# Performance work log

Measured on AMD Instinct MI355X. Metric: run time of the kernel, lower is better.

## Reference

```python
import jax, jax.numpy as jnp
import numpy as np
import math

NUM_LABELS = 8
D_MODEL = 1024
NUM_HEADS = 16
D_PADDED = math.ceil(D_MODEL / NUM_HEADS) * NUM_HEADS  # 1024
D_HEAD = D_PADDED // NUM_HEADS  # 64
B, N = 4, 2048


def setup_inputs() -> dict:
    key = jax.random.key(0)
    ks = jax.random.split(key, 7)
    X = jax.random.normal(ks[0], (B, N, D_MODEL), dtype=jnp.float32)
    L = jax.random.randint(ks[1], (B, N), 0, NUM_LABELS, dtype=jnp.int32)
    # per-label QKV linear params (stored as x @ W + b layout)
    s_in = 1.0 / math.sqrt(D_MODEL)
    Wqkv = jax.random.uniform(ks[2], (NUM_LABELS, D_MODEL, 3 * D_PADDED), jnp.float32, -s_in, s_in)
    bqkv = jax.random.uniform(ks[3], (NUM_LABELS, 3 * D_PADDED), jnp.float32, -s_in, s_in)
    s_p = 1.0 / math.sqrt(D_PADDED)
    Wproj = jax.random.uniform(ks[4], (D_PADDED, D_MODEL), jnp.float32, -s_p, s_p)
    bproj = jax.random.uniform(ks[5], (D_MODEL,), jnp.float32, -s_p, s_p)
    return {"X": X, "L": L, "Wqkv": Wqkv, "bqkv": bqkv, "Wproj": Wproj, "bproj": bproj}


def reference(X, L, Wqkv, bqkv, Wproj, bproj):
    Bb, Nn, _ = X.shape
    # Per-label dense QKV projection, routed by label mask (matches original
    # per-label loop; X_masked zeroing is a no-op on selected positions).
    qkv = jnp.zeros((Bb, Nn, 3 * D_PADDED), dtype=X.dtype)
    for l in range(NUM_LABELS):
        m = (L == l)[..., None]  # [B, N, 1]
        qkv_l = jnp.einsum('bnd,do->bno', X, Wqkv[l]) + bqkv[l]
        qkv = jnp.where(m, qkv_l, qkv)
    q, k, v = jnp.split(qkv, 3, axis=-1)
    # [B, H, N, Dh]
    q = q.reshape(Bb, Nn, NUM_HEADS, D_HEAD).transpose(0, 2, 1, 3)
    k = k.reshape(Bb, Nn, NUM_HEADS, D_HEAD).transpose(0, 2, 1, 3)
    v = v.reshape(Bb, Nn, NUM_HEADS, D_HEAD).transpose(0, 2, 1, 3)
    scores = jnp.einsum('bhnd,bhmd->bhnm', q, k) / math.sqrt(D_HEAD)
    probs = jax.nn.softmax(scores, axis=-1)
    out = jnp.einsum('bhnm,bhmd->bhnd', probs, v)
    out = out.transpose(0, 2, 1, 3).reshape(Bb, Nn, D_PADDED)
    return jnp.einsum('bnd,do->bno', out, Wproj) + bproj
```

## Files before the change

kernel.cpp:

```cpp
#include <hip/hip_runtime.h>
#include <math.h>

#define BATCH 4
#define SEQ   2048
#define TOK   (BATCH * SEQ)
#define DM    1024
#define DP    1024
#define NH    16
#define DH    64
#define NLAB  8
#define QKV_C 3072
#define PADL  1152
#define PROWS (NLAB * PADL)
#define GP    72

typedef __attribute__((ext_vector_type(8))) short bf16x8;
typedef __attribute__((ext_vector_type(4))) float f32x4;

__device__ __forceinline__ short f2bf(float f) {
  union { float f; unsigned u; } v; v.f = f;
  unsigned r = v.u + 0x7FFF + ((v.u >> 16) & 1);
  return (short)(r >> 16);
}

__device__ __forceinline__ unsigned cvt_pk_bf16(float lo, float hi) {
  unsigned r;
  asm("v_cvt_pk_bf16_f32 %0, %1, %2" : "=v"(r) : "v"(lo), "v"(hi));
  return r;
}

__device__ __forceinline__ float fast_exp2(float x) {
#if __has_builtin(__builtin_amdgcn_exp2f)
  return __builtin_amdgcn_exp2f(x);
#else
  return exp2f(x);
#endif
}

__global__ void build_lists_k(const int* __restrict__ L, int* __restrict__ sorted,
                              int* __restrict__ rowmap) {
  __shared__ int cnt[NLAB], off[NLAB], cur[NLAB];
  int tid = threadIdx.x;
  if (tid < NLAB) cnt[tid] = 0;
  __syncthreads();
  for (int i = tid; i < TOK; i += 256) atomicAdd(&cnt[L[i]], 1);
  __syncthreads();
  if (tid == 0) {
    int o = 0;
    for (int l = 0; l < NLAB; ++l) { off[l] = o; cur[l] = o; o += cnt[l]; }
  }
  __syncthreads();
  for (int i = tid; i < TOK; i += 256) {
    int l = L[i];
    sorted[atomicAdd(&cur[l], 1)] = i;
  }
  __threadfence();
  __syncthreads();
  for (int p = tid; p < PROWS; p += 256) {
    int l = p / PADL, i = p - l * PADL;
    rowmap[p] = (i < cnt[l]) ? sorted[off[l] + i] : -1;
  }
}

__global__ __launch_bounds__(256) void xg_k(const float* __restrict__ X,
                                            const int* __restrict__ rowmap,
                                            short* __restrict__ Xg) {
  int p = blockIdx.x;
  int t = rowmap[p];
  int c = threadIdx.x << 2;
  short* dst = Xg + (size_t)p * DM + c;
  if (t >= 0) {
    float4 v = *(const float4*)(X + (size_t)t * DM + c);
    short tmp[4] = { f2bf(v.x), f2bf(v.y), f2bf(v.z), f2bf(v.w) };
    *(uint2*)dst = *(uint2*)tmp;
  } else {
    uint2 z; z.x = 0u; z.y = 0u;
    *(uint2*)dst = z;
  }
}

__global__ __launch_bounds__(256) void wt_k(const float* __restrict__ src,
                                            short* __restrict__ dst,
                                            int K, int N) {
  __shared__ float Ts[64][65];
  int m = blockIdx.z;
  src += (size_t)m * K * N;
  dst += (size_t)m * (size_t)N * K;
  int n0 = blockIdx.x * 64, k0 = blockIdx.y * 64;
  int tid = threadIdx.x;
  int r = tid >> 4;
  int c = (tid & 15) << 2;
  #pragma unroll
  for (int it = 0; it < 4; ++it) {
    float4 v = *(const float4*)(src + (size_t)(k0 + r + it * 16) * N + n0 + c);
    Ts[c + 0][r + it * 16] = v.x;
    Ts[c + 1][r + it * 16] = v.y;
    Ts[c + 2][r + it * 16] = v.z;
    Ts[c + 3][r + it * 16] = v.w;
  }
  __syncthreads();
  int n = tid >> 2, ks = (tid & 3) << 4;
  short tmp[16];
  #pragma unroll
  for (int j = 0; j < 16; ++j) tmp[j] = f2bf(Ts[n][ks + j]);
  *(bf16x8*)(dst + (size_t)(n0 + n) * K + k0 + ks)     = *(bf16x8*)&tmp[0];
  *(bf16x8*)(dst + (size_t)(n0 + n) * K + k0 + ks + 8) = *(bf16x8*)&tmp[8];
}

__global__ __launch_bounds__(256) void qkv_mfma_k(
    const short* __restrict__ Xg, const short* __restrict__ Wt,
    const float* __restrict__ bqkv, const int* __restrict__ rowmap,
    short* __restrict__ qkvb) {
  __shared__ short As[128 * GP];
  __shared__ short Bs[128 * GP];
  int bx = blockIdx.x, by = blockIdx.y;
  int lab = by / 9;
  int pr0 = by * 128;
  int n0  = bx * 128;
  const short* W = Wt + (size_t)lab * QKV_C * DM;

  int tid  = threadIdx.x;
  int lane = tid & 63, w = tid >> 6;
  int wm = w >> 1, wn = w & 1;
  int col = lane & 15, quad = lane >> 4;

  int srow = tid >> 2;
  int scol = (tid & 3) << 4;

  const short* a0 = Xg + (size_t)(pr0 + srow) * DM + scol;
  const short* a1 = Xg + (size_t)(pr0 + 64 + srow) * DM + scol;
  const short* b0 = W + (size_t)(n0 + srow) * DM + scol;
  const short* b1 = W + (size_t)(n0 + 64 + srow) * DM + scol;

  f32x4 acc[4][4];
  #pragma unroll
  for (int mi = 0; mi < 4; ++mi)
    #pragma unroll
    for (int ni = 0; ni < 4; ++ni) acc[mi][ni] = (f32x4){0.f, 0.f, 0.f, 0.f};

  bf16x8 ra[4], rb[4];
  ra[0] = *(const bf16x8*)(a0);     ra[1] = *(const bf16x8*)(a0 + 8);
  ra[2] = *(const bf16x8*)(a1);     ra[3] = *(const bf16x8*)(a1 + 8);
  rb[0] = *(const bf16x8*)(b0);     rb[1] = *(const bf16x8*)(b0 + 8);
  rb[2] = *(const bf16x8*)(b1);     rb[3] = *(const bf16x8*)(b1 + 8);

  for (int k0 = 0; k0 < DM; k0 += 64) {
    *(bf16x8*)&As[srow * GP + scol]            = ra[0];
    *(bf16x8*)&As[srow * GP + scol + 8]        = ra[1];
    *(bf16x8*)&As[(64 + srow) * GP + scol]     = ra[2];
    *(bf16x8*)&As[(64 + srow) * GP + scol + 8] = ra[3];
    *(bf16x8*)&Bs[srow * GP + scol]            = rb[0];
    *(bf16x8*)&Bs[srow * GP + scol + 8]        = rb[1];
    *(bf16x8*)&Bs[(64 + srow) * GP + scol]     = rb[2];
    *(bf16x8*)&Bs[(64 + srow) * GP + scol + 8] = rb[3];
    __syncthreads();
    if (k0 + 64 < DM) {
      int kn = k0 + 64;
      ra[0] = *(const bf16x8*)(a0 + kn);     ra[1] = *(const bf16x8*)(a0 + kn + 8);
      ra[2] = *(const bf16x8*)(a1 + kn);     ra[3] = *(const bf16x8*)(a1 + kn + 8);
      rb[0] = *(const bf16x8*)(b0 + kn);     rb[1] = *(const bf16x8*)(b0 + kn + 8);
      rb[2] = *(const bf16x8*)(b1 + kn);     rb[3] = *(const bf16x8*)(b1 + kn + 8);
    }
    #pragma unroll
    for (int ks = 0; ks < 2; ++ks) {
      bf16x8 a[4], b[4];
      #pragma unroll
      for (int mi = 0; mi < 4; ++mi)
        a[mi] = *(bf16x8*)&As[(wm * 64 + mi * 16 + col) * GP + ks * 32 + (quad << 3)];
      #pragma unroll
      for (int ni = 0; ni < 4; ++ni)
        b[ni] = *(bf16x8*)&Bs[(wn * 64 + ni * 16 + col) * GP + ks * 32 + (quad << 3)];
      #pragma unroll
      for (int mi = 0; mi < 4; ++mi)
        #pragma unroll
        for (int ni = 0; ni < 4; ++ni)
          acc[mi][ni] = __builtin_amdgcn_mfma_f32_16x16x32_bf16(a[mi], b[ni], acc[mi][ni], 0, 0, 0);
    }
    __syncthreads();
  }

  float scale = (bx < 8) ? (0.125f * 1.44269504f) : 1.0f;
  const float* bias = bqkv + lab * QKV_C;
  #pragma unroll
  for (int mi = 0; mi < 4; ++mi) {
    #pragma unroll
    for (int r = 0; r < 4; ++r) {
      int prow = pr0 + wm * 64 + mi * 16 + (quad << 2) + r;
      int t2 = rowmap[prow];
      if (t2 < 0) continue;
      #pragma unroll
      for (int ni = 0; ni < 4; ++ni) {
        int gn = n0 + wn * 64 + ni * 16 + col;
        float v = (acc[mi][ni][r] + bias[gn]) * scale;
        qkvb[(size_t)t2 * QKV_C + gn] = f2bf(v);
      }
    }
  }
}

__global__ __launch_bounds__(256) void vtb_k(const short* __restrict__ qkvb,
                                             short* __restrict__ VTg) {
  __shared__ short T[64 * GP];
  int n0 = blockIdx.x * 64, h = blockIdx.y, b = blockIdx.z;
  int tid = threadIdx.x;
  int r = tid >> 2, cb = tid & 3;
  {
    const short* src = qkvb + ((size_t)(b * SEQ + n0 + r)) * QKV_C + 2 * DP + h * DH + (cb << 4);
    int scc = ((cb + (r >> 4)) & 3) << 4;
    *(bf16x8*)&T[r * GP + scc]     = *(const bf16x8*)(src);
    *(bf16x8*)&T[r * GP + scc + 8] = *(const bf16x8*)(src + 8);
  }
  __syncthreads();
  int d = tid >> 2, nc = (tid & 3) << 4;
  int sc2 = (((d >> 4) + (nc >> 4)) & 3) << 4;
  short tmp[16];
  #pragma unroll
  for (int j = 0; j < 16; ++j) tmp[j] = T[(nc + j) * GP + sc2 + (d & 15)];
  short* dst = VTg + ((size_t)(b * NH + h) * DH + d) * SEQ + n0 + nc;
  *(bf16x8*)&dst[0] = *(bf16x8*)&tmp[0];
  *(bf16x8*)&dst[8] = *(bf16x8*)&tmp[8];
}

__global__ __launch_bounds__(256) void attn_k(short* __restrict__ qkvb,
                                              const short* __restrict__ VTg) {
  int qt = blockIdx.x, h = blockIdx.y, b = blockIdx.z;
  __shared__ short Ks[64 * GP];
  __shared__ short VT[64 * GP];
  __shared__ short Ps[128 * GP];

  int tid  = threadIdx.x;
  int lane = tid & 63;
  int w    = tid >> 6;
  int col  = lane & 15;
  int quad = lane >> 4;

  size_t rowbase = (size_t)b * SEQ;
  int hoff = h * DH;
  int sr = tid >> 2;
  int sc = (tid & 3) << 4;

  const short* ksrc = qkvb + (rowbase + sr) * QKV_C + DP + hoff + sc;
  const short* vsrc = VTg + ((size_t)(b * NH + h) * DH + sr) * SEQ + sc;

  bf16x8 qf0[2], qf1[2];
  {
    const short* q0 = qkvb + (rowbase + qt * 128 + (w << 4) + col) * QKV_C + hoff + (quad << 3);
    const short* q1 = q0 + (size_t)64 * QKV_C;
    qf0[0] = *(const bf16x8*)(q0);
    qf0[1] = *(const bf16x8*)(q0 + 32);
    qf1[0] = *(const bf16x8*)(q1);
    qf1[1] = *(const bf16x8*)(q1 + 32);
  }

  {
    bf16x8 ka = *(const bf16x8*)(ksrc);
    bf16x8 kb = *(const bf16x8*)(ksrc + 8);
    bf16x8 va = *(const bf16x8*)(vsrc);
    bf16x8 vb = *(const bf16x8*)(vsrc + 8);
    *(bf16x8*)&Ks[sr * GP + sc]     = ka;
    *(bf16x8*)&Ks[sr * GP + sc + 8] = kb;
    *(bf16x8*)&VT[sr * GP + sc]     = va;
    *(bf16x8*)&VT[sr * GP + sc + 8] = vb;
  }
  __syncthreads();

  float m_0 = -1e30f, l_0 = 0.f, m_1 = -1e30f, l_1 = 0.f;
  f32x4 o0[4], o1[4];
  #pragma unroll
  for (int nd = 0; nd < 4; ++nd) {
    o0[nd] = (f32x4){0.f, 0.f, 0.f, 0.f};
    o1[nd] = (f32x4){0.f, 0.f, 0.f, 0.f};
  }

  short* ps0 = &Ps[((w << 4) + col) * GP];
  short* ps1 = &Ps[(64 + (w << 4) + col) * GP];

  auto softmax_strip = [&](f32x4* s, float& m_, float& l_, f32x4* o, short* psrow) {
    f32x4 t0, t1;
    #pragma unroll
    for (int i = 0; i < 4; ++i) { t0[i] = fmaxf(s[0][i], s[1][i]); t1[i] = fmaxf(s[2][i], s[3][i]); }
    #pragma unroll
    for (int i = 0; i < 4; ++i) t0[i] = fmaxf(t0[i], t1[i]);
    float mx = fmaxf(fmaxf(t0[0], t0[1]), fmaxf(t0[2], t0[3]));
    if (!__all(mx - m_ <= 8.f)) {
      float mxr = fmaxf(mx, __shfl_xor(mx, 16));
      mxr = fmaxf(mxr, __shfl_xor(mxr, 32));
      float mnew  = fmaxf(m_, mxr);
      float alpha = fast_exp2(m_ - mnew);
      l_ *= alpha;
      #pragma unroll
      for (int nd = 0; nd < 4; ++nd)
        #pragma unroll
        for (int r = 0; r < 4; ++r) o[nd][r] *= alpha;
      m_ = mnew;
    }
    float p[4][4];
    #pragma unroll
    for (int nj = 0; nj < 4; ++nj)
      #pragma unroll
      for (int r = 0; r < 4; ++r) p[nj][r] = fast_exp2(s[nj][r] - m_);
    float rs = 0.f;
    #pragma unroll
    for (int nj = 0; nj < 4; ++nj)
      rs += (p[nj][0] + p[nj][1]) + (p[nj][2] + p[nj][3]);
    l_ += rs;
    #pragma unroll
    for (int nj = 0; nj < 4; ++nj) {
      uint2 u;
      u.x = cvt_pk_bf16(p[nj][0], p[nj][1]);
      u.y = cvt_pk_bf16(p[nj][2], p[nj][3]);
      *(uint2*)&psrow[nj * 16 + (quad << 2)] = u;
    }
  };

  auto compute_tile = [&]() {
    f32x4 s0[4], s1[4];
    #pragma unroll
    for (int nj = 0; nj < 4; ++nj) {
      s0[nj] = (f32x4){0.f, 0.f, 0.f, 0.f};
      s1[nj] = (f32x4){0.f, 0.f, 0.f, 0.f};
    }
    __builtin_amdgcn_s_setprio(1);
    #pragma unroll
    for (int ks = 0; ks < 2; ++ks) {
      #pragma unroll
      for (int nj = 0; nj < 4; ++nj) {
        bf16x8 aK = *(bf16x8*)&Ks[((nj << 4) + col) * GP + (ks << 5) + (quad << 3)];
        s0[nj] = __builtin_amdgcn_mfma_f32_16x16x32_bf16(aK, qf0[ks], s0[nj], 0, 0, 0);
        s1[nj] = __builtin_amdgcn_mfma_f32_16x16x32_bf16(aK, qf1[ks], s1[nj], 0, 0, 0);
      }
    }
    __builtin_amdgcn_s_setprio(0);
    softmax_strip(s0, m_0, l_0, o0, ps0);
    softmax_strip(s1, m_1, l_1, o1, ps1);
    __builtin_amdgcn_s_setprio(1);
    #pragma unroll
    for (int ks = 0; ks < 2; ++ks) {
      bf16x8 bP0 = *(bf16x8*)&ps0[(ks << 5) + (quad << 3)];
      bf16x8 bP1 = *(bf16x8*)&ps1[(ks << 5) + (quad << 3)];
      #pragma unroll
      for (int nd = 0; nd < 4; ++nd) {
        bf16x8 aV = *(bf16x8*)&VT[((nd << 4) + col) * GP + (ks << 5) + (quad << 3)];
        o0[nd] = __builtin_amdgcn_mfma_f32_16x16x32_bf16(aV, bP0, o0[nd], 0, 0, 0);
        o1[nd] = __builtin_amdgcn_mfma_f32_16x16x32_bf16(aV, bP1, o1[nd], 0, 0, 0);
      }
    }
    __builtin_amdgcn_s_setprio(0);
  };

  for (int kt = 0; kt < SEQ / 64 - 1; ++kt) {
    const short* kn = ksrc + (size_t)(kt + 1) * 64 * QKV_C;
    const short* vn = vsrc + (size_t)(kt + 1) * 64;
    bf16x8 ka = *(const bf16x8*)(kn);
    bf16x8 kb = *(const bf16x8*)(kn + 8);
    bf16x8 va = *(const bf16x8*)(vn);
    bf16x8 vb = *(const bf16x8*)(vn + 8);

    compute_tile();
    __syncthreads();
    *(bf16x8*)&Ks[sr * GP + sc]     = ka;
    *(bf16x8*)&Ks[sr * GP + sc + 8] = kb;
    *(bf16x8*)&VT[sr * GP + sc]     = va;
    *(bf16x8*)&VT[sr * GP + sc + 8] = vb;
    __syncthreads();
  }
  compute_tile();

  float lt0 = l_0 + __shfl_xor(l_0, 16);
  lt0 += __shfl_xor(lt0, 32);
  float lt1 = l_1 + __shfl_xor(l_1, 16);
  lt1 += __shfl_xor(lt1, 32);
  #pragma unroll
  for (int s = 0; s < 2; ++s) {
    float inv = 1.f / (s ? lt1 : lt0);
    f32x4* o = s ? o1 : o0;
    size_t row = rowbase + qt * 128 + s * 64 + (w << 4) + col;
    #pragma unroll
    for (int nd = 0; nd < 4; ++nd) {
      uint2 u;
      u.x = cvt_pk_bf16(o[nd][0] * inv, o[nd][1] * inv);
      u.y = cvt_pk_bf16(o[nd][2] * inv, o[nd][3] * inv);
      *(uint2*)(qkvb + row * QKV_C + hoff + (nd << 4) + (quad << 2)) = u;
    }
  }
}

__global__ __launch_bounds__(256) void proj_mfma_k(
    const short* __restrict__ Ab, const short* __restrict__ Wt,
    const float* __restrict__ bias, float* __restrict__ out) {
  __shared__ short As[128 * GP];
  __shared__ short Bs[128 * GP];
  int n0 = blockIdx.x * 128, m0 = blockIdx.y * 128;

  int tid  = threadIdx.x;
  int lane = tid & 63, w = tid >> 6;
  int wm = w >> 1, wn = w & 1;
  int col = lane & 15, quad = lane >> 4;
  int srow = tid >> 2;
  int scol = (tid & 3) << 4;

  const short* a0 = Ab + (size_t)(m0 + srow) * QKV_C + scol;
  const short* a1 = Ab + (size_t)(m0 + 64 + srow) * QKV_C + scol;
  const short* b0 = Wt + (size_t)(n0 + srow) * DP + scol;
  const short* b1 = Wt + (size_t)(n0 + 64 + srow) * DP + scol;

  f32x4 acc[4][4];
  #pragma unroll
  for (int mi = 0; mi < 4; ++mi)
    #pragma unroll
    for (int ni = 0; ni < 4; ++ni) acc[mi][ni] = (f32x4){0.f, 0.f, 0.f, 0.f};

  bf16x8 ra[4], rb[4];
  ra[0] = *(const bf16x8*)(a0);     ra[1] = *(const bf16x8*)(a0 + 8);
  ra[2] = *(const bf16x8*)(a1);     ra[3] = *(const bf16x8*)(a1 + 8);
  rb[0] = *(const bf16x8*)(b0);     rb[1] = *(const bf16x8*)(b0 + 8);
  rb[2] = *(const bf16x8*)(b1);     rb[3] = *(const bf16x8*)(b1 + 8);

  for (int k0 = 0; k0 < DP; k0 += 64) {
    *(bf16x8*)&As[srow * GP + scol]            = ra[0];
    *(bf16x8*)&As[srow * GP + scol + 8]        = ra[1];
    *(bf16x8*)&As[(64 + srow) * GP + scol]     = ra[2];
    *(bf16x8*)&As[(64 + srow) * GP + scol + 8] = ra[3];
    *(bf16x8*)&Bs[srow * GP + scol]            = rb[0];
    *(bf16x8*)&Bs[srow * GP + scol + 8]        = rb[1];
    *(bf16x8*)&Bs[(64 + srow) * GP + scol]     = rb[2];
    *(bf16x8*)&Bs[(64 + srow) * GP + scol + 8] = rb[3];
    __syncthreads();
    if (k0 + 64 < DP) {
      int kn = k0 + 64;
      ra[0] = *(const bf16x8*)(a0 + kn);     ra[1] = *(const bf16x8*)(a0 + kn + 8);
      ra[2] = *(const bf16x8*)(a1 + kn);     ra[3] = *(const bf16x8*)(a1 + kn + 8);
      rb[0] = *(const bf16x8*)(b0 + kn);     rb[1] = *(const bf16x8*)(b0 + kn + 8);
      rb[2] = *(const bf16x8*)(b1 + kn);     rb[3] = *(const bf16x8*)(b1 + kn + 8);
    }
    #pragma unroll
    for (int ks = 0; ks < 2; ++ks) {
      bf16x8 a[4], b[4];
      #pragma unroll
      for (int mi = 0; mi < 4; ++mi)
        a[mi] = *(bf16x8*)&As[(wm * 64 + mi * 16 + col) * GP + ks * 32 + (quad << 3)];
      #pragma unroll
      for (int ni = 0; ni < 4; ++ni)
        b[ni] = *(bf16x8*)&Bs[(wn * 64 + ni * 16 + col) * GP + ks * 32 + (quad << 3)];
      #pragma unroll
      for (int mi = 0; mi < 4; ++mi)
        #pragma unroll
        for (int ni = 0; ni < 4; ++ni)
          acc[mi][ni] = __builtin_amdgcn_mfma_f32_16x16x32_bf16(a[mi], b[ni], acc[mi][ni], 0, 0, 0);
    }
    __syncthreads();
  }

  #pragma unroll
  for (int mi = 0; mi < 4; ++mi) {
    #pragma unroll
    for (int r = 0; r < 4; ++r) {
      int m = m0 + wm * 64 + mi * 16 + (quad << 2) + r;
      #pragma unroll
      for (int ni = 0; ni < 4; ++ni) {
        int gn = n0 + wn * 64 + ni * 16 + col;
        out[(size_t)m * DM + gn] = acc[mi][ni][r] + bias[gn];
      }
    }
  }
}

extern "C" void kernel_launch(void* const* d_in, const int* in_sizes, int n_in,
                              void* d_out, int out_size, void* d_ws, size_t ws_size,
                              hipStream_t stream) {
  (void)in_sizes; (void)n_in; (void)out_size; (void)ws_size;
  const float* X     = (const float*)d_in[0];
  const int*   L     = (const int*)d_in[1];
  const float* Wqkv  = (const float*)d_in[2];
  const float* bqkv  = (const float*)d_in[3];
  const float* Wproj = (const float*)d_in[4];
  const float* bproj = (const float*)d_in[5];
  float* out = (float*)d_out;

  char* ws = (char*)d_ws;
  short* qkvb    = (short*)ws;
  short* Wqkv_t  = (short*)(ws + (size_t)TOK * QKV_C * 2);
  short* Wproj_t = (short*)(ws + (size_t)TOK * QKV_C * 2
                               + (size_t)NLAB * QKV_C * DM * 2);
  int* sorted = (int*)((char*)Wproj_t + (size_t)DP * DM * 2);
  int* rowmap = sorted + TOK;
  short* Xg = (short*)(rowmap + PROWS);
  short* VTg = Wqkv_t;

  build_lists_k<<<dim3(1), dim3(256), 0, stream>>>(L, sorted, rowmap);
  xg_k<<<dim3(PROWS), dim3(256), 0, stream>>>(X, rowmap, Xg);
  wt_k<<<dim3(QKV_C / 64, DM / 64, NLAB), dim3(256), 0, stream>>>(Wqkv, Wqkv_t, DM, QKV_C);
  wt_k<<<dim3(DM / 64, DP / 64, 1), dim3(256), 0, stream>>>(Wproj, Wproj_t, DP, DM);
  qkv_mfma_k<<<dim3(QKV_C / 128, PROWS / 128), dim3(256), 0, stream>>>(
      Xg, Wqkv_t, bqkv, rowmap, qkvb);
  vtb_k<<<dim3(SEQ / 64, NH, BATCH), dim3(256), 0, stream>>>(qkvb, VTg);
  attn_k<<<dim3(SEQ / 128, NH, BATCH), dim3(256), 0, stream>>>(qkvb, VTg);
  proj_mfma_k<<<dim3(DM / 128, TOK / 128), dim3(256), 0, stream>>>(
      qkvb, Wproj_t, bproj, out);
}
```

Measured before the change: 458.7 us.

## Load GEMM tiles directly into LDS with global_load_lds in QKV and proj kernels

Both MFMA GEMM kernels now stage A and B tiles with global_load_lds (direct global-to-LDS DMA) instead of loading into registers and writing to padded shared memory. The register prefetch of the next tile is removed, and the LDS layout drops its padding to an unpadded 64-element row stride. This cuts VGPR pressure and the extra ds_write instructions. In exchange the loads are no longer overlapped with MFMA work, since the kernel syncs right after issuing them, and the unpadded layout may cause LDS bank conflicts on the fragment reads.

```diff
diff --git a/kernel.cpp b/kernel.cpp
--- a/kernel.cpp
+++ b/kernel.cpp
@@ -16,6 +16,9 @@
 
 typedef __attribute__((ext_vector_type(8))) short bf16x8;
 typedef __attribute__((ext_vector_type(4))) float f32x4;
+
+typedef const __attribute__((address_space(1))) void* gas_ptr;
+typedef __attribute__((address_space(3))) void* las_ptr;
 
 __device__ __forceinline__ short f2bf(float f) {
   union { float f; unsigned u; } v; v.f = f;
@@ -111,8 +114,8 @@
     const short* __restrict__ Xg, const short* __restrict__ Wt,
     const float* __restrict__ bqkv, const int* __restrict__ rowmap,
     short* __restrict__ qkvb) {
-  __shared__ short As[128 * GP];
-  __shared__ short Bs[128 * GP];
+  __shared__ short As[128 * 64];
+  __shared__ short Bs[128 * 64];
   int bx = blockIdx.x, by = blockIdx.y;
   int lab = by / 9;
   int pr0 = by * 128;
@@ -124,13 +127,11 @@
   int wm = w >> 1, wn = w & 1;
   int col = lane & 15, quad = lane >> 4;
 
-  int srow = tid >> 2;
-  int scol = (tid & 3) << 4;
-
-  const short* a0 = Xg + (size_t)(pr0 + srow) * DM + scol;
-  const short* a1 = Xg + (size_t)(pr0 + 64 + srow) * DM + scol;
-  const short* b0 = W + (size_t)(n0 + srow) * DM + scol;
-  const short* b1 = W + (size_t)(n0 + 64 + srow) * DM + scol;
+  int lrow = lane >> 3;
+  int lcol = (lane & 7) << 3;
+
+  const short* aSrc = Xg + (size_t)(pr0 + w * 32 + lrow) * DM + lcol;
+  const short* bSrc = W  + (size_t)(n0  + w * 32 + lrow) * DM + lcol;
 
   f32x4 acc[4][4];
   #pragma unroll
@@ -138,45 +139,33 @@
     #pragma unroll
     for (int ni = 0; ni < 4; ++ni) acc[mi][ni] = (f32x4){0.f, 0.f, 0.f, 0.f};
 
-  bf16x8 ra[4], rb[4];
-  ra[0] = *(const bf16x8*)(a0);     ra[1] = *(const bf16x8*)(a0 + 8);
-  ra[2] = *(const bf16x8*)(a1);     ra[3] = *(const bf16x8*)(a1 + 8);
-  rb[0] = *(const bf16x8*)(b0);     rb[1] = *(const bf16x8*)(b0 + 8);
-  rb[2] = *(const bf16x8*)(b1);     rb[3] = *(const bf16x8*)(b1 + 8);
-
   for (int k0 = 0; k0 < DM; k0 += 64) {
-    *(bf16x8*)&As[srow * GP + scol]            = ra[0];
-    *(bf16x8*)&As[srow * GP + scol + 8]        = ra[1];
-    *(bf16x8*)&As[(64 + srow) * GP + scol]     = ra[2];
-    *(bf16x8*)&As[(64 + srow) * GP + scol + 8] = ra[3];
-    *(bf16x8*)&Bs[srow * GP + scol]            = rb[0];
-    *(bf16x8*)&Bs[srow * GP + scol + 8]        = rb[1];
-    *(bf16x8*)&Bs[(64 + srow) * GP + scol]     = rb[2];
-    *(bf16x8*)&Bs[(64 + srow) * GP + scol + 8] = rb[3];
-    __syncthreads();
-    if (k0 + 64 < DM) {
-      int kn = k0 + 64;
-      ra[0] = *(const bf16x8*)(a0 + kn);     ra[1] = *(const bf16x8*)(a0 + kn + 8);
-      ra[2] = *(const bf16x8*)(a1 + kn);     ra[3] = *(const bf16x8*)(a1 + kn + 8);
-      rb[0] = *(const bf16x8*)(b0 + kn);     rb[1] = *(const bf16x8*)(b0 + kn + 8);
-      rb[2] = *(const bf16x8*)(b1 + kn);     rb[3] = *(const bf16x8*)(b1 + kn + 8);
-    }
+    __syncthreads();
+    #pragma unroll
+    for (int it = 0; it < 4; ++it) {
+      __builtin_amdgcn_global_load_lds(
+          (gas_ptr)(aSrc + (size_t)(it * 8) * DM + k0),
+          (las_ptr)&As[(w * 32 + it * 8) * 64], 16, 0, 0);
+      __builtin_amdgcn_global_load_lds(
+          (gas_ptr)(bSrc + (size_t)(it * 8) * DM + k0),
+          (las_ptr)&Bs[(w * 32 + it * 8) * 64], 16, 0, 0);
+    }
+    __syncthreads();
     #pragma unroll
     for (int ks = 0; ks < 2; ++ks) {
       bf16x8 a[4], b[4];
       #pragma unroll
       for (int mi = 0; mi < 4; ++mi)
-        a[mi] = *(bf16x8*)&As[(wm * 64 + mi * 16 + col) * GP + ks * 32 + (quad << 3)];
+        a[mi] = *(bf16x8*)&As[(wm * 64 + mi * 16 + col) * 64 + ks * 32 + (quad << 3)];
       #pragma unroll
       for (int ni = 0; ni < 4; ++ni)
-        b[ni] = *(bf16x8*)&Bs[(wn * 64 + ni * 16 + col) * GP + ks * 32 + (quad << 3)];
+        b[ni] = *(bf16x8*)&Bs[(wn * 64 + ni * 16 + col) * 64 + ks * 32 + (quad << 3)];
       #pragma unroll
       for (int mi = 0; mi < 4; ++mi)
         #pragma unroll
         for (int ni = 0; ni < 4; ++ni)
           acc[mi][ni] = __builtin_amdgcn_mfma_f32_16x16x32_bf16(a[mi], b[ni], acc[mi][ni], 0, 0, 0);
     }
-    __syncthreads();
   }
 
   float scale = (bx < 8) ? (0.125f * 1.44269504f) : 1.0f;
@@ -388,21 +377,20 @@
 __global__ __launch_bounds__(256) void proj_mfma_k(
     const short* __restrict__ Ab, const short* __restrict__ Wt,
     const float* __restrict__ bias, float* __restrict__ out) {
-  __shared__ short As[128 * GP];
-  __shared__ short Bs[128 * GP];
+  __shared__ short As[128 * 64];
+  __shared__ short Bs[128 * 64];
   int n0 = blockIdx.x * 128, m0 = blockIdx.y * 128;
 
   int tid  = threadIdx.x;
   int lane = tid & 63, w = tid >> 6;
   int wm = w >> 1, wn = w & 1;
   int col = lane & 15, quad = lane >> 4;
-  int srow = tid >> 2;
-  int scol = (tid & 3) << 4;
-
-  const short* a0 = Ab + (size_t)(m0 + srow) * QKV_C + scol;
-  const short* a1 = Ab + (size_t)(m0 + 64 + srow) * QKV_C + scol;
-  const short* b0 = Wt + (size_t)(n0 + srow) * DP + scol;
-  const short* b1 = Wt + (size_t)(n0 + 64 + srow) * DP + scol;
+
+  int lrow = lane >> 3;
+  int lcol = (lane & 7) << 3;
+
+  const short* aSrc = Ab + (size_t)(m0 + w * 32 + lrow) * QKV_C + lcol;
+  const short* bSrc = Wt + (size_t)(n0 + w * 32 + lrow) * DP + lcol;
 
   f32x4 acc[4][4];
   #pragma unroll
@@ -410,45 +398,33 @@
     #pragma unroll
     for (int ni = 0; ni < 4; ++ni) acc[mi][ni] = (f32x4){0.f, 0.f, 0.f, 0.f};
 
-  bf16x8 ra[4], rb[4];
-  ra[0] = *(const bf16x8*)(a0);     ra[1] = *(const bf16x8*)(a0 + 8);
-  ra[2] = *(const bf16x8*)(a1);     ra[3] = *(const bf16x8*)(a1 + 8);
-  rb[0] = *(const bf16x8*)(b0);     rb[1] = *(const bf16x8*)(b0 + 8);
-  rb[2] = *(const bf16x8*)(b1);     rb[3] = *(const bf16x8*)(b1 + 8);
-
   for (int k0 = 0; k0 < DP; k0 += 64) {
-    *(bf16x8*)&As[srow * GP + scol]            = ra[0];
-    *(bf16x8*)&As[srow * GP + scol + 8]        = ra[1];
-    *(bf16x8*)&As[(64 + srow) * GP + scol]     = ra[2];
-    *(bf16x8*)&As[(64 + srow) * GP + scol + 8] = ra[3];
-    *(bf16x8*)&Bs[srow * GP + scol]            = rb[0];
-    *(bf16x8*)&Bs[srow * GP + scol + 8]        = rb[1];
-    *(bf16x8*)&Bs[(64 + srow) * GP + scol]     = rb[2];
-    *(bf16x8*)&Bs[(64 + srow) * GP + scol + 8] = rb[3];
-    __syncthreads();
-    if (k0 + 64 < DP) {
-      int kn = k0 + 64;
-      ra[0] = *(const bf16x8*)(a0 + kn);     ra[1] = *(const bf16x8*)(a0 + kn + 8);
-      ra[2] = *(const bf16x8*)(a1 + kn);     ra[3] = *(const bf16x8*)(a1 + kn + 8);
-      rb[0] = *(const bf16x8*)(b0 + kn);     rb[1] = *(const bf16x8*)(b0 + kn + 8);
-      rb[2] = *(const bf16x8*)(b1 + kn);     rb[3] = *(const bf16x8*)(b1 + kn + 8);
-    }
+    __syncthreads();
+    #pragma unroll
+    for (int it = 0; it < 4; ++it) {
+      __builtin_amdgcn_global_load_lds(
+          (gas_ptr)(aSrc + (size_t)(it * 8) * QKV_C + k0),
+          (las_ptr)&As[(w * 32 + it * 8) * 64], 16, 0, 0);
+      __builtin_amdgcn_global_load_lds(
+          (gas_ptr)(bSrc + (size_t)(it * 8) * DP + k0),
+          (las_ptr)&Bs[(w * 32 + it * 8) * 64], 16, 0, 0);
+    }
+    __syncthreads();
     #pragma unroll
     for (int ks = 0; ks < 2; ++ks) {
       bf16x8 a[4], b[4];
       #pragma unroll
       for (int mi = 0; mi < 4; ++mi)
-        a[mi] = *(bf16x8*)&As[(wm * 64 + mi * 16 + col) * GP + ks * 32 + (quad << 3)];
+        a[mi] = *(bf16x8*)&As[(wm * 64 + mi * 16 + col) * 64 + ks * 32 + (quad << 3)];
       #pragma unroll
       for (int ni = 0; ni < 4; ++ni)
-        b[ni] = *(bf16x8*)&Bs[(wn * 64 + ni * 16 + col) * GP + ks * 32 + (quad << 3)];
+        b[ni] = *(bf16x8*)&Bs[(wn * 64 + ni * 16 + col) * 64 + ks * 32 + (quad << 3)];
       #pragma unroll
       for (int mi = 0; mi < 4; ++mi)
         #pragma unroll
         for (int ni = 0; ni < 4; ++ni)
           acc[mi][ni] = __builtin_amdgcn_mfma_f32_16x16x32_bf16(a[mi], b[ni], acc[mi][ni], 0, 0, 0);
     }
-    __syncthreads();
   }
 
   #pragma unroll
```

Result: slower. 481.6 us (+5.0%).
